# Performance work log

Measured on AMD Instinct MI355X. Metric: run time of the kernel, lower is better.

## Reference

```python
import jax, jax.numpy as jnp
import numpy as np

B, P, D, S = 1024, 200, 512, 64  # batch, num prototypes (nall), feat_dim, subdim


def setup_inputs() -> dict:
    key = jax.random.key(0)
    k1, k2, k3 = jax.random.split(key, 3)
    x = jax.random.normal(k1, (B, D), dtype=jnp.float32)
    protos = jax.random.normal(k2, (P, D), dtype=jnp.float32)
    subspaces = jax.random.normal(k3, (P, D, S), dtype=jnp.float32)
    return {"x": x, "protos": protos, "subspaces": subspaces}


def reference(x, protos, subspaces):
    # diff: [B, P, D]
    diff = x[:, None, :] - protos[None, :, :]
    # per-prototype tangent-space projectors: I - U U^T, [P, D, D]
    projectors = jnp.eye(D, dtype=subspaces.dtype) - jnp.einsum(
        'pds,pes->pde', subspaces, subspaces)
    # project diffs and take L2 norm over feature dim -> [B, P]
    proj_diff = jnp.einsum('bpd,pde->bpe', diff, projectors)
    return jnp.linalg.norm(proj_diff, ord=2, axis=-1)
```

## Files before the change

kernel.cpp:

```cpp
#include <hip/hip_runtime.h>
#include <math.h>


#define NB 1024
#define NP 200
#define ND 512
#define NS 64
#define NS5 80

#define OFF_C   0
#define OFF_PN  12800
#define OFF_XN  13000
#define OFF_GB  14024
#define OFF_XB  423624
#define OFF_UB  685768

typedef __attribute__((ext_vector_type(8))) short bf16x8;
typedef __attribute__((ext_vector_type(8))) unsigned short ushort8;
typedef __attribute__((ext_vector_type(4))) float f32x4;

__device__ __forceinline__ unsigned short f2bf(float f) {
  unsigned int u = __float_as_uint(f);
  u += 0x7fffu + ((u >> 16) & 1u);
  return (unsigned short)(u >> 16);
}
__device__ __forceinline__ float bf2f(unsigned short h) {
  return __uint_as_float(((unsigned int)h) << 16);
}
__device__ __forceinline__ void gl_lds16(const void* g, void* l) {
  __builtin_amdgcn_global_load_lds(
      (const __attribute__((address_space(1))) unsigned int*)g,
      (__attribute__((address_space(3))) unsigned int*)l, 16, 0, 0);
}

__global__ __launch_bounds__(256) void k_conv(
    const float* __restrict__ x, const float* __restrict__ protos,
    const float* __restrict__ U, float* __restrict__ ws)
{
  const int bid = blockIdx.x, tid = threadIdx.x;
  if (bid >= 800) {
    const int b = (bid - 800) * 32 + (tid >> 3);
    const int cc = tid & 7;
    const float* src = x + (size_t)b * ND + cc * 64;
    unsigned short* dst = (unsigned short*)(ws + OFF_XB) + (size_t)b * ND + cc * 64;
    float s = 0.f;
#pragma unroll
    for (int i = 0; i < 8; ++i) {
      float4 v0 = *(const float4*)(src + i * 8);
      float4 v1 = *(const float4*)(src + i * 8 + 4);
      ushort8 o;
      o[0]=f2bf(v0.x); o[1]=f2bf(v0.y); o[2]=f2bf(v0.z); o[3]=f2bf(v0.w);
      o[4]=f2bf(v1.x); o[5]=f2bf(v1.y); o[6]=f2bf(v1.z); o[7]=f2bf(v1.w);
      *(ushort8*)(dst + i * 8) = o;
      s += v0.x*v0.x + v0.y*v0.y + v0.z*v0.z + v0.w*v0.w
         + v1.x*v1.x + v1.y*v1.y + v1.z*v1.z + v1.w*v1.w;
    }
    s += __shfl_xor(s, 1); s += __shfl_xor(s, 2); s += __shfl_xor(s, 4);
    if (cc == 0) ws[OFF_XN + b] = s;
    return;
  }
  const int p = bid >> 2, d0 = (bid & 3) * 128;
  __shared__ unsigned short ts[128][66];
#pragma unroll
  for (int i = 0; i < 8; ++i) {
    int row = (tid >> 4) + i * 16;
    int col = (tid & 15) * 4;
    float4 v = *(const float4*)(U + ((size_t)p * ND + d0 + row) * NS + col);
    ts[row][col] = f2bf(v.x); ts[row][col+1] = f2bf(v.y);
    ts[row][col+2] = f2bf(v.z); ts[row][col+3] = f2bf(v.w);
  }
  __syncthreads();
  unsigned short* Ubg = (unsigned short*)(ws + OFF_UB) + (size_t)p * NS5 * ND;
#pragma unroll
  for (int i = 0; i < 4; ++i) {
    int f = tid + i * 256;
    int s = f >> 4, g = f & 15;
    ushort8 o;
#pragma unroll
    for (int j = 0; j < 8; ++j) o[j] = ts[g * 8 + j][s];
    *(ushort8*)(Ubg + (size_t)s * ND + d0 + g * 8) = o;
  }
  if (tid < 16) {
    const float* pr = protos + (size_t)p * ND + d0 + tid * 8;
    float4 v0 = *(const float4*)pr, v1 = *(const float4*)(pr + 4);
    ushort8 o;
    o[0]=f2bf(v0.x); o[1]=f2bf(v0.y); o[2]=f2bf(v0.z); o[3]=f2bf(v0.w);
    o[4]=f2bf(v1.x); o[5]=f2bf(v1.y); o[6]=f2bf(v1.z); o[7]=f2bf(v1.w);
    *(ushort8*)(Ubg + (size_t)64 * ND + d0 + tid * 8) = o;
  }
}

__global__ __launch_bounds__(256) void k_gram(float* __restrict__ ws) {
  const int p = blockIdx.x;
  __shared__ __align__(16) unsigned short ut[NS5 * ND];
  const int tid = threadIdx.x, l = tid & 63, w = tid >> 6;
  const int lm = l & 15, lh = l >> 4;
  const unsigned short* ub =
      (const unsigned short*)(ws + OFF_UB) + (size_t)p * NS5 * ND;
#pragma unroll
  for (int i = 0; i < 20; ++i) {
    int f = tid + i * 256;
    int r = f >> 6;
    int gd = (f & 63) ^ (r & 15);
    *(ushort8*)(ut + (size_t)f * 8) = *(const ushort8*)(ub + (size_t)r * ND + gd * 8);
  }
  __syncthreads();
  const int ntile = (w == 0) ? 6 : 5;
  for (int idx = 0; idx < ntile; ++idx) {
    int tt = (idx == 5) ? 20 : (w + 4 * idx);
    int i1 = (tt == 20) ? 4 : tt / 5;
    int i2 = (tt == 20) ? 4 : tt % 5;
    f32x4 g = {0.f, 0.f, 0.f, 0.f};
#pragma unroll
    for (int ks = 0; ks < 16; ++ks) {
      int sl = (ks * 4 + lh) ^ lm;
      bf16x8 a = *(const bf16x8*)(ut + ((size_t)(i1 * 16 + lm) * 64 + sl) * 8);
      bf16x8 b = *(const bf16x8*)(ut + ((size_t)(i2 * 16 + lm) * 64 + sl) * 8);
      g = __builtin_amdgcn_mfma_f32_16x16x32_bf16(a, b, g, 0, 0, 0);
    }
    int col = i2 * 16 + lm;
    int row0 = i1 * 16 + lh * 4;
    if (i1 < 4 && i2 < 4) {
      unsigned short* Gbg = (unsigned short*)(ws + OFF_GB) + (size_t)p * 4096;
#pragma unroll
      for (int q = 0; q < 4; ++q) Gbg[(size_t)(row0 + q) * 64 + col] = f2bf(g[q]);
    } else if (i1 < 4 && i2 == 4 && lm == 0) {
#pragma unroll
      for (int q = 0; q < 4; ++q) ws[OFF_C + p * 64 + row0 + q] = g[q];
    } else if (tt == 20 && l == 0) {
      ws[OFF_PN + p] = g[0];
    }
  }
}

__global__ __launch_bounds__(256, 2) void k_main(float* __restrict__ ws,
                                                 float* __restrict__ out)
{
  const int p = blockIdx.x;
  const int b0 = blockIdx.y * 128;
  __shared__ __align__(16) unsigned short ut[72 * 512];
  unsigned short* tb = ut;
  const int tid = threadIdx.x, l = tid & 63, w = tid >> 6;
  const int lm = l & 15, lh = l >> 4;

  const unsigned short* Xb = (const unsigned short*)(ws + OFF_XB) + (size_t)b0 * ND;
  const unsigned short* Ub = (const unsigned short*)(ws + OFF_UB) + (size_t)p * NS5 * ND;
  const unsigned short* Gbg = (const unsigned short*)(ws + OFF_GB) + (size_t)p * 4096;

#pragma unroll
  for (int i = 0; i < 18; ++i) {
    int f = i * 256 + w * 64 + l;
    int r = f >> 6, gd = (f & 63) ^ (r & 15);
    gl_lds16(Ub + (size_t)r * ND + gd * 8, ut + (size_t)(i * 256 + w * 64) * 8);
  }
  float cr[4];
#pragma unroll
  for (int j = 0; j < 4; ++j) cr[j] = ws[OFF_C + p * 64 + j * 16 + lm];

  asm volatile("s_waitcnt vmcnt(0) lgkmcnt(0)" ::: "memory");
  __builtin_amdgcn_s_barrier();

  const unsigned short* xr0 = Xb + (size_t)((w * 2 + 0) * 16 + lm) * ND;
  const unsigned short* xr1 = Xb + (size_t)((w * 2 + 1) * 16 + lm) * ND;
  f32x4 acc[2][5] = {};
#pragma unroll
  for (int it = 0; it < 8; ++it) {
#pragma unroll
    for (int ks = 0; ks < 2; ++ks) {
      const int gd = it * 8 + ks * 4 + lh;
      bf16x8 a0 = *(const bf16x8*)(xr0 + gd * 8);
      bf16x8 a1 = *(const bf16x8*)(xr1 + gd * 8);
#pragma unroll
      for (int j = 0; j < 4; ++j) {
        const int r = j * 16 + lm;
        bf16x8 b = *(const bf16x8*)(ut + (size_t)(r * 64 + (gd ^ lm)) * 8);
        acc[0][j] = __builtin_amdgcn_mfma_f32_16x16x32_bf16(a0, b, acc[0][j], 0, 0, 0);
        acc[1][j] = __builtin_amdgcn_mfma_f32_16x16x32_bf16(a1, b, acc[1][j], 0, 0, 0);
      }
      {
        const int r = 64 + (lm & 7);
        bf16x8 b = *(const bf16x8*)(ut + (size_t)(r * 64 + (gd ^ (lm & 7))) * 8);
        acc[0][4] = __builtin_amdgcn_mfma_f32_16x16x32_bf16(a0, b, acc[0][4], 0, 0, 0);
        acc[1][4] = __builtin_amdgcn_mfma_f32_16x16x32_bf16(a1, b, acc[1][4], 0, 0, 0);
      }
    }
  }

  bf16x8 gfrag[2][4];
#pragma unroll
  for (int ks = 0; ks < 2; ++ks)
#pragma unroll
    for (int j = 0; j < 4; ++j)
      gfrag[ks][j] = *(const bf16x8*)(Gbg + (size_t)(j * 16 + lm) * 64 + ks * 32 + lh * 8);

  __syncthreads();

  float tn[2][4] = {};
  float xpr[2][4];
#pragma unroll
  for (int i = 0; i < 2; ++i) {
    int rbase = (w * 2 + i) * 16 + lh * 4;
#pragma unroll
    for (int j = 0; j < 4; ++j) {
      f32x4 v = acc[i][j];
      int col = j * 16 + lm;
#pragma unroll
      for (int q = 0; q < 4; ++q) {
        float t = v[q] - cr[j];
        tn[i][q] += t * t;
        tb[(size_t)(rbase + q) * 72 + col] = f2bf(t);
      }
    }
#pragma unroll
    for (int q = 0; q < 4; ++q) xpr[i][q] = acc[i][4][q];
  }

  f32x4 acc2[2][4] = {};
#pragma unroll
  for (int ks = 0; ks < 2; ++ks)
#pragma unroll
    for (int i = 0; i < 2; ++i) {
      bf16x8 a = *(const bf16x8*)(tb + (size_t)((w*2+i)*16 + lm) * 72 + ks*32 + lh*8);
#pragma unroll
      for (int j = 0; j < 4; ++j)
        acc2[i][j] = __builtin_amdgcn_mfma_f32_16x16x32_bf16(a, gfrag[ks][j], acc2[i][j], 0, 0, 0);
    }

  const float pnv = ws[OFF_PN + p];
#pragma unroll
  for (int i = 0; i < 2; ++i) {
    int rbase = (w * 2 + i) * 16 + lh * 4;
    float tgt[4] = {0.f, 0.f, 0.f, 0.f};
#pragma unroll
    for (int j = 0; j < 4; ++j) {
      int col = j * 16 + lm;
#pragma unroll
      for (int q = 0; q < 4; ++q)
        tgt[q] += acc2[i][j][q] * bf2f(tb[(size_t)(rbase + q) * 72 + col]);
    }
#pragma unroll
    for (int q = 0; q < 4; ++q) {
      float ta = tgt[q], tnv = tn[i][q];
#pragma unroll
      for (int m = 1; m <= 8; m <<= 1) {
        ta += __shfl_xor(ta, m);
        tnv += __shfl_xor(tnv, m);
      }
      tgt[q] = ta; tn[i][q] = tnv;
    }
    if (lm == 0) {
#pragma unroll
      for (int q = 0; q < 4; ++q) {
        int r = rbase + q;
        int bb = b0 + r;
        float qq = ws[OFF_XN + bb] - 2.f * xpr[i][q] + pnv;
        float v = qq - 2.f * tn[i][q] + tgt[q];
        out[(size_t)bb * NP + p] = sqrtf(fmaxf(v, 0.f));
      }
    }
  }
}

extern "C" void kernel_launch(void* const* d_in, const int* in_sizes, int n_in,
                              void* d_out, int out_size, void* d_ws, size_t ws_size,
                              hipStream_t stream) {
  const float* x      = (const float*)d_in[0];
  const float* protos = (const float*)d_in[1];
  const float* U      = (const float*)d_in[2];
  float* out = (float*)d_out;
  float* ws  = (float*)d_ws;

  k_conv<<<dim3(832),   dim3(256), 0, stream>>>(x, protos, U, ws);
  k_gram<<<dim3(NP),    dim3(256), 0, stream>>>(ws);
  k_main<<<dim3(NP, 8), dim3(256), 0, stream>>>(ws, out);
}
```

Baseline: 130.7 us.

## Halve LDS staging of subspace tile and prefetch X fragments to raise occupancy

The U tile is now staged into LDS in two halves along the feature dimension, with a barrier and restage between them. This halves shared memory per block so launch bounds can request three blocks per SIMD instead of two. X fragments are software-prefetched two k-steps ahead in a three-deep register ring. The cost is an extra barrier and a serialized reload in the middle of the GEMM loop, plus added register pressure that may conflict with the higher occupancy target.

```diff
diff --git a/kernel.cpp b/kernel.cpp
--- a/kernel.cpp
+++ b/kernel.cpp
@@ -133,12 +133,12 @@
   }
 }
 
-__global__ __launch_bounds__(256, 2) void k_main(float* __restrict__ ws,
+__global__ __launch_bounds__(256, 3) void k_main(float* __restrict__ ws,
                                                  float* __restrict__ out)
 {
   const int p = blockIdx.x;
   const int b0 = blockIdx.y * 128;
-  __shared__ __align__(16) unsigned short ut[72 * 512];
+  __shared__ __align__(16) unsigned short ut[72 * 256];
   unsigned short* tb = ut;
   const int tid = threadIdx.x, l = tid & 63, w = tid >> 6;
   const int lm = l & 15, lh = l >> 4;
@@ -147,42 +147,64 @@
   const unsigned short* Ub = (const unsigned short*)(ws + OFF_UB) + (size_t)p * NS5 * ND;
   const unsigned short* Gbg = (const unsigned short*)(ws + OFF_GB) + (size_t)p * 4096;
 
-#pragma unroll
-  for (int i = 0; i < 18; ++i) {
-    int f = i * 256 + w * 64 + l;
-    int r = f >> 6, gd = (f & 63) ^ (r & 15);
-    gl_lds16(Ub + (size_t)r * ND + gd * 8, ut + (size_t)(i * 256 + w * 64) * 8);
-  }
+  auto stageHalf = [&](int h) {
+#pragma unroll
+    for (int i = 0; i < 9; ++i) {
+      int f = i * 256 + w * 64 + l;
+      int r = f >> 5, gd = (f & 31) ^ (r & 15);
+      gl_lds16(Ub + (size_t)r * ND + h * 256 + gd * 8,
+               ut + (size_t)(i * 256 + w * 64) * 8);
+    }
+  };
+
+  const unsigned short* xr0 = Xb + (size_t)((w * 2 + 0) * 16 + lm) * ND;
+  const unsigned short* xr1 = Xb + (size_t)((w * 2 + 1) * 16 + lm) * ND;
+
+  stageHalf(0);
   float cr[4];
 #pragma unroll
   for (int j = 0; j < 4; ++j) cr[j] = ws[OFF_C + p * 64 + j * 16 + lm];
+
+  bf16x8 pa0[3], pa1[3];
+  pa0[0] = *(const bf16x8*)(xr0 + (0 * 4 + lh) * 8);
+  pa1[0] = *(const bf16x8*)(xr1 + (0 * 4 + lh) * 8);
+  pa0[1] = *(const bf16x8*)(xr0 + (1 * 4 + lh) * 8);
+  pa1[1] = *(const bf16x8*)(xr1 + (1 * 4 + lh) * 8);
 
   asm volatile("s_waitcnt vmcnt(0) lgkmcnt(0)" ::: "memory");
   __builtin_amdgcn_s_barrier();
 
-  const unsigned short* xr0 = Xb + (size_t)((w * 2 + 0) * 16 + lm) * ND;
-  const unsigned short* xr1 = Xb + (size_t)((w * 2 + 1) * 16 + lm) * ND;
   f32x4 acc[2][5] = {};
 #pragma unroll
-  for (int it = 0; it < 8; ++it) {
-#pragma unroll
-    for (int ks = 0; ks < 2; ++ks) {
-      const int gd = it * 8 + ks * 4 + lh;
-      bf16x8 a0 = *(const bf16x8*)(xr0 + gd * 8);
-      bf16x8 a1 = *(const bf16x8*)(xr1 + gd * 8);
+  for (int h = 0; h < 2; ++h) {
+#pragma unroll
+    for (int s = 0; s < 8; ++s) {
+      const int u = h * 8 + s;
+      if (u < 14) {
+        pa0[(u + 2) % 3] = *(const bf16x8*)(xr0 + ((u + 2) * 4 + lh) * 8);
+        pa1[(u + 2) % 3] = *(const bf16x8*)(xr1 + ((u + 2) * 4 + lh) * 8);
+      }
+      const int sl = s * 4 + lh;
+      bf16x8 a0 = pa0[u % 3], a1 = pa1[u % 3];
 #pragma unroll
       for (int j = 0; j < 4; ++j) {
         const int r = j * 16 + lm;
-        bf16x8 b = *(const bf16x8*)(ut + (size_t)(r * 64 + (gd ^ lm)) * 8);
+        bf16x8 b = *(const bf16x8*)(ut + (size_t)(r * 32 + (sl ^ lm)) * 8);
         acc[0][j] = __builtin_amdgcn_mfma_f32_16x16x32_bf16(a0, b, acc[0][j], 0, 0, 0);
         acc[1][j] = __builtin_amdgcn_mfma_f32_16x16x32_bf16(a1, b, acc[1][j], 0, 0, 0);
       }
       {
         const int r = 64 + (lm & 7);
-        bf16x8 b = *(const bf16x8*)(ut + (size_t)(r * 64 + (gd ^ (lm & 7))) * 8);
+        bf16x8 b = *(const bf16x8*)(ut + (size_t)(r * 32 + (sl ^ (lm & 7))) * 8);
         acc[0][4] = __builtin_amdgcn_mfma_f32_16x16x32_bf16(a0, b, acc[0][4], 0, 0, 0);
         acc[1][4] = __builtin_amdgcn_mfma_f32_16x16x32_bf16(a1, b, acc[1][4], 0, 0, 0);
       }
+    }
+    if (h == 0) {
+      __builtin_amdgcn_s_barrier();
+      stageHalf(1);
+      asm volatile("s_waitcnt vmcnt(0)" ::: "memory");
+      __builtin_amdgcn_s_barrier();
     }
   }
 
```

Measured after the change: 128.6 us. No clear change (-1.6%).
